# Optimization experiments

Hardware: AMD Instinct MI355X
Metric: run time of the kernel (lower is better)

## Reference

```python
import jax, jax.numpy as jnp
import numpy as np

N = 50000      # nodes
E = 800000     # edges (avg degree 16)
S = 2          # sample_size
D_IN = 128     # input_dim
D_NOISE = 64   # noise_dim
D0 = 256       # output_dims[0]
D1 = 256       # output_dims[1]


def setup_inputs() -> dict:
    key = jax.random.key(0)
    ks = jax.random.split(key, 8)
    X = jax.random.normal(ks[0], (1, N, D_IN), dtype=jnp.float32)
    edge_src = jax.random.randint(ks[1], (E,), 0, N)
    edge_dst = jax.random.randint(ks[2], (E,), 0, N)
    # Bernoulli(0.5) noise, as in torch.distributions.Bernoulli
    epsilon = (jax.random.uniform(ks[3], (S, N, D_NOISE)) < 0.5).astype(jnp.float32)
    W0 = jax.random.normal(ks[4], (D_IN + D_NOISE, D0), dtype=jnp.float32) * 0.05
    b0 = jnp.zeros((D0,), jnp.float32)
    W1 = jax.random.normal(ks[5], (D0, D1), dtype=jnp.float32) * 0.05
    b1 = jnp.zeros((D1,), jnp.float32)
    eps0 = jnp.zeros((), jnp.float32)  # GINConv learnable eps, init 0
    eps1 = jnp.zeros((), jnp.float32)
    return dict(X=X, epsilon=epsilon, edge_src=edge_src, edge_dst=edge_dst,
                W0=W0, b0=b0, W1=W1, b1=b1, eps0=eps0, eps1=eps1)


def reference(X, epsilon, edge_src, edge_dst, W0, b0, W1, b1, eps0, eps1):
    # Expand features over sample dim and concat noise: [S, N, D_IN + D_NOISE]
    feat = jnp.broadcast_to(X, (epsilon.shape[0], X.shape[1], X.shape[2]))
    h = jnp.concatenate([feat, epsilon], axis=2)

    def gin_layer(h, eps, W, b):
        # sum aggregation over in-edges: agg[:, d] += h[:, s] for each edge (s, d)
        agg = jnp.zeros_like(h).at[:, edge_dst, :].add(h[:, edge_src, :])
        return jax.nn.relu(((1.0 + eps) * h + agg) @ W + b)

    h = gin_layer(h, eps0, W0, b0)
    h = gin_layer(h, eps1, W1, b1)
    out = jax.nn.relu(h)  # outer activation applied once more in forward()
    return out, epsilon
```

## Files before the change

kernel.cpp:

```cpp
#include <hip/hip_runtime.h>
#include <hip/hip_bf16.h>

#define NN 50000
#define NE 800000
#define NS 2
#define DIN 128
#define DNOISE 64
#define DH0 192
#define DOUT 256

typedef __bf16 bf16x8 __attribute__((ext_vector_type(8)));
typedef float floatx4 __attribute__((ext_vector_type(4)));


__global__ void count_kernel(const int* __restrict__ dst, int* __restrict__ cnt) {
    int i = blockIdx.x * blockDim.x + threadIdx.x;
    if (i < NE) atomicAdd(&cnt[dst[i]], 1);
}

__global__ __launch_bounds__(1024) void scan_kernel(int* __restrict__ cnt ,
                                                    int* __restrict__ row_ptr) {
    __shared__ int buf[1024];
    __shared__ int carry_s;
    int tid = threadIdx.x;
    if (tid == 0) { carry_s = 0; row_ptr[0] = 0; }
    __syncthreads();
    for (int base = 0; base < NN; base += 1024) {
        int i = base + tid;
        int v = (i < NN) ? cnt[i] : 0;
        buf[tid] = v;
        __syncthreads();
        for (int off = 1; off < 1024; off <<= 1) {
            int t = (tid >= off) ? buf[tid - off] : 0;
            __syncthreads();
            buf[tid] += t;
            __syncthreads();
        }
        int inc = buf[tid] + carry_s;
        if (i < NN) { row_ptr[i + 1] = inc; cnt[i] = inc - v; }
        __syncthreads();
        if (tid == 1023) carry_s = inc;
        __syncthreads();
    }
}

__global__ void fill_kernel(const int* __restrict__ src, const int* __restrict__ dst,
                            int* __restrict__ cursor, int* __restrict__ col_idx) {
    int i = blockIdx.x * blockDim.x + threadIdx.x;
    if (i < NE) {
        int p = atomicAdd(&cursor[dst[i]], 1);
        col_idx[p] = src[i];
    }
}


__global__ void transpose_w(const float* __restrict__ W, __hip_bfloat16* __restrict__ Wt, int K) {
    int n = blockIdx.x;
    for (int k = threadIdx.x; k < K; k += blockDim.x)
        Wt[(size_t)n * K + k] = __float2bfloat16(W[(size_t)k * DOUT + n]);
}


__device__ inline float bflo(unsigned int u) { return __uint_as_float(u << 16); }
__device__ inline float bfhi(unsigned int u) { return __uint_as_float(u & 0xffff0000u); }
__device__ inline unsigned short f2bf_bits(float x) {
    __hip_bfloat16 b = __float2bfloat16(x);
    return *reinterpret_cast<unsigned short*>(&b);
}


__global__ __launch_bounds__(256) void agg0_kernel(
    const float* __restrict__ X, const float* __restrict__ noise,
    const int* __restrict__ row_ptr, const int* __restrict__ col_idx,
    const float* __restrict__ eps0p, __hip_bfloat16* __restrict__ z0) {
    int d = blockIdx.x, tid = threadIdx.x;
    int beg = row_ptr[d], end = row_ptr[d + 1];
    float c = 1.f + eps0p[0];
    if (tid < DIN) {
        const float* src = X + tid;
        float acc = c * src[(size_t)d * DIN];
        int e = beg;
        for (; e + 3 < end; e += 4) {
            int i0 = col_idx[e], i1 = col_idx[e + 1], i2 = col_idx[e + 2], i3 = col_idx[e + 3];
            float v0 = src[(size_t)i0 * DIN], v1 = src[(size_t)i1 * DIN];
            float v2 = src[(size_t)i2 * DIN], v3 = src[(size_t)i3 * DIN];
            acc += (v0 + v1) + (v2 + v3);
        }
        for (; e < end; ++e) acc += src[(size_t)col_idx[e] * DIN];
        __hip_bfloat16 r = __float2bfloat16(acc);
        z0[(size_t)d * DH0 + tid] = r;
        z0[(size_t)(NN + d) * DH0 + tid] = r;
    } else {
        int j = tid - DIN;
        int s = j >> 6, dim = j & 63;
        const float* src = noise + (size_t)s * NN * DNOISE + dim;
        float acc = c * src[(size_t)d * DNOISE];
        int e = beg;
        for (; e + 3 < end; e += 4) {
            int i0 = col_idx[e], i1 = col_idx[e + 1], i2 = col_idx[e + 2], i3 = col_idx[e + 3];
            float v0 = src[(size_t)i0 * DNOISE], v1 = src[(size_t)i1 * DNOISE];
            float v2 = src[(size_t)i2 * DNOISE], v3 = src[(size_t)i3 * DNOISE];
            acc += (v0 + v1) + (v2 + v3);
        }
        for (; e < end; ++e) acc += src[(size_t)col_idx[e] * DNOISE];
        z0[(size_t)(s * NN + d) * DH0 + DIN + dim] = __float2bfloat16(acc);
    }
}


__global__ __launch_bounds__(256) void agg1_kernel(
    const unsigned int* __restrict__ h, const int* __restrict__ row_ptr,
    const int* __restrict__ col_idx, const float* __restrict__ eps1p,
    unsigned int* __restrict__ z1) {
    const int RW = DOUT / 2;
    int d = blockIdx.x, tid = threadIdx.x;
    int s = tid >> 7, cidx = tid & 127;
    int beg = row_ptr[d], end = row_ptr[d + 1];
    float c = 1.f + eps1p[0];
    const unsigned int* src = h + (size_t)s * NN * RW + cidx;
    unsigned int u = src[(size_t)d * RW];
    float aL = c * bflo(u), aH = c * bfhi(u);
    int e = beg;
    for (; e + 3 < end; e += 4) {
        int i0 = col_idx[e], i1 = col_idx[e + 1], i2 = col_idx[e + 2], i3 = col_idx[e + 3];
        unsigned int u0 = src[(size_t)i0 * RW], u1 = src[(size_t)i1 * RW];
        unsigned int u2 = src[(size_t)i2 * RW], u3 = src[(size_t)i3 * RW];
        aL += (bflo(u0) + bflo(u1)) + (bflo(u2) + bflo(u3));
        aH += (bfhi(u0) + bfhi(u1)) + (bfhi(u2) + bfhi(u3));
    }
    for (; e < end; ++e) {
        unsigned int ue = src[(size_t)col_idx[e] * RW];
        aL += bflo(ue); aH += bfhi(ue);
    }
    z1[(size_t)(s * NN + d) * RW + cidx] =
        (unsigned int)f2bf_bits(aL) | ((unsigned int)f2bf_bits(aH) << 16);
}


__device__ inline void store_out(float* C, size_t idx, float v) { C[idx] = v; }
__device__ inline void store_out(__hip_bfloat16* C, size_t idx, float v) { C[idx] = __float2bfloat16(v); }

template <typename OUT_T>
__global__ __launch_bounds__(256) void gemm_bias_relu(
    const __hip_bfloat16* __restrict__ A, const __hip_bfloat16* __restrict__ Wt,
    const float* __restrict__ bias, OUT_T* __restrict__ C,
    int M, int K) {
    const int lane = threadIdx.x & 63;
    const int wave = threadIdx.x >> 6;
    const int rowBase = blockIdx.x * 128 + wave * 32;
    if (rowBase >= M) return;
    const int lo = lane & 15;
    const int quad = lane >> 4;

    floatx4 acc0[16], acc1[16];
#pragma unroll
    for (int t = 0; t < 16; ++t) {
        acc0[t] = (floatx4){0.f, 0.f, 0.f, 0.f};
        acc1[t] = (floatx4){0.f, 0.f, 0.f, 0.f};
    }

    const __hip_bfloat16* arow0 = A + (size_t)(rowBase + lo) * K + quad * 8;
    const __hip_bfloat16* arow1 = arow0 + (size_t)16 * K;
    for (int k0 = 0; k0 < K; k0 += 32) {
        bf16x8 a0 = *reinterpret_cast<const bf16x8*>(arow0 + k0);
        bf16x8 a1 = *reinterpret_cast<const bf16x8*>(arow1 + k0);
#pragma unroll
        for (int t = 0; t < 16; ++t) {
            bf16x8 b = *reinterpret_cast<const bf16x8*>(Wt + (size_t)(t * 16 + lo) * K + k0 + quad * 8);
            acc0[t] = __builtin_amdgcn_mfma_f32_16x16x32_bf16(a0, b, acc0[t], 0, 0, 0);
            acc1[t] = __builtin_amdgcn_mfma_f32_16x16x32_bf16(a1, b, acc1[t], 0, 0, 0);
        }
    }

#pragma unroll
    for (int t = 0; t < 16; ++t) {
        int col = t * 16 + lo;
        float bv = bias[col];
#pragma unroll
        for (int r = 0; r < 4; ++r) {
            int row0 = rowBase + quad * 4 + r;
            float v0 = acc0[t][r] + bv;
            store_out(C, (size_t)row0 * DOUT + col, v0 > 0.f ? v0 : 0.f);
            float v1 = acc1[t][r] + bv;
            store_out(C, (size_t)(row0 + 16) * DOUT + col, v1 > 0.f ? v1 : 0.f);
        }
    }
}


__global__ void copy_eps(const uint4* __restrict__ src, uint4* __restrict__ dst) {
    int i = blockIdx.x * blockDim.x + threadIdx.x;
    const int n16 = (NS * NN * DNOISE * 4) / 16;
    if (i < n16) dst[i] = src[i];
}

extern "C" void kernel_launch(void* const* d_in, const int* in_sizes, int n_in,
                              void* d_out, int out_size, void* d_ws, size_t ws_size,
                              hipStream_t stream) {
    const float* X = (const float*)d_in[0];
    const float* noise = (const float*)d_in[1];
    const int* esrc = (const int*)d_in[2];
    const int* edst = (const int*)d_in[3];
    const float* W0 = (const float*)d_in[4];
    const float* b0 = (const float*)d_in[5];
    const float* W1 = (const float*)d_in[6];
    const float* b1 = (const float*)d_in[7];
    const float* eps0 = (const float*)d_in[8];
    const float* eps1 = (const float*)d_in[9];
    float* out = (float*)d_out;

    char* w = (char*)d_ws;
    auto carve = [&](size_t bytes) { char* p = w; w += (bytes + 511) & ~(size_t)511; return p; };
    int* cursor = (int*)carve((size_t)NN * 4);
    int* row_ptr = (int*)carve((size_t)(NN + 1) * 4);
    int* col_idx = (int*)carve((size_t)NE * 4);
    __hip_bfloat16* Wt0 = (__hip_bfloat16*)carve((size_t)DH0 * DOUT * 2);
    __hip_bfloat16* Wt1 = (__hip_bfloat16*)carve((size_t)DOUT * DOUT * 2);
    __hip_bfloat16* z = (__hip_bfloat16*)carve((size_t)NS * NN * DOUT * 2);
    __hip_bfloat16* h1 = (__hip_bfloat16*)d_out;

    const int M = NS * NN;

    hipMemsetAsync(cursor, 0, (size_t)NN * 4, stream);
    count_kernel<<<(NE + 255) / 256, 256, 0, stream>>>(edst, cursor);
    scan_kernel<<<1, 1024, 0, stream>>>(cursor, row_ptr);
    fill_kernel<<<(NE + 255) / 256, 256, 0, stream>>>(esrc, edst, cursor, col_idx);
    transpose_w<<<DOUT, 256, 0, stream>>>(W0, Wt0, DH0);
    transpose_w<<<DOUT, 256, 0, stream>>>(W1, Wt1, DOUT);

    agg0_kernel<<<NN, 256, 0, stream>>>(X, noise, row_ptr, col_idx, eps0, z);
    gemm_bias_relu<__hip_bfloat16><<<(M + 127) / 128, 256, 0, stream>>>(z, Wt0, b0, h1, M, DH0);
    agg1_kernel<<<NN, 256, 0, stream>>>((const unsigned int*)h1, row_ptr, col_idx, eps1,
                                        (unsigned int*)z);
    gemm_bias_relu<float><<<(M + 127) / 128, 256, 0, stream>>>(z, Wt1, b1, out, M, DOUT);

    copy_eps<<<((NS * NN * DNOISE * 4 / 16) + 255) / 256, 256, 0, stream>>>(
        (const uint4*)noise, (uint4*)(out + (size_t)M * DOUT));
}
```

Baseline: 708.0 us.

## Fuse neighbor aggregation with MFMA GEMM per 32-node tile and gather bf16 inputs

Each GIN layer's aggregation and GEMM are merged into one kernel. A block of 32 nodes gathers neighbor sums for both samples into shared memory, then runs bf16 MFMA with bias and ReLU, so the aggregated intermediate is never written to or read back from global memory. X and the noise are first converted to bf16, using the epsilon output area as scratch, to halve the bytes each gather moves, and the scan now processes four counts per thread. The trade-offs are a serial per-node loop inside each block, which means less parallelism for gathers, and rounding the inputs to bf16 before aggregation.

```diff
diff --git a/kernel.cpp b/kernel.cpp
--- a/kernel.cpp
+++ b/kernel.cpp
@@ -13,6 +13,17 @@
 typedef float floatx4 __attribute__((ext_vector_type(4)));
 
 
+__device__ inline float bflo(unsigned int u) { return __uint_as_float(u << 16); }
+__device__ inline float bfhi(unsigned int u) { return __uint_as_float(u & 0xffff0000u); }
+__device__ inline unsigned short f2bf_bits(float x) {
+    __hip_bfloat16 b = __float2bfloat16(x);
+    return *reinterpret_cast<unsigned short*>(&b);
+}
+__device__ inline unsigned int pack2(float lo, float hi) {
+    return (unsigned int)f2bf_bits(lo) | ((unsigned int)f2bf_bits(hi) << 16);
+}
+
+
 __global__ void count_kernel(const int* __restrict__ dst, int* __restrict__ cnt) {
     int i = blockIdx.x * blockDim.x + threadIdx.x;
     if (i < NE) atomicAdd(&cnt[dst[i]], 1);
@@ -25,10 +36,20 @@
     int tid = threadIdx.x;
     if (tid == 0) { carry_s = 0; row_ptr[0] = 0; }
     __syncthreads();
-    for (int base = 0; base < NN; base += 1024) {
-        int i = base + tid;
-        int v = (i < NN) ? cnt[i] : 0;
-        buf[tid] = v;
+    for (int base = 0; base < NN; base += 4096) {
+        int i = base + tid * 4;
+        int v0 = 0, v1 = 0, v2 = 0, v3 = 0;
+        if (i + 3 < NN) {
+            int4 q = *reinterpret_cast<const int4*>(cnt + i);
+            v0 = q.x; v1 = q.y; v2 = q.z; v3 = q.w;
+        } else {
+            if (i < NN) v0 = cnt[i];
+            if (i + 1 < NN) v1 = cnt[i + 1];
+            if (i + 2 < NN) v2 = cnt[i + 2];
+            if (i + 3 < NN) v3 = cnt[i + 3];
+        }
+        int s = v0 + v1 + v2 + v3;
+        buf[tid] = s;
         __syncthreads();
         for (int off = 1; off < 1024; off <<= 1) {
             int t = (tid >= off) ? buf[tid - off] : 0;
@@ -36,10 +57,14 @@
             buf[tid] += t;
             __syncthreads();
         }
-        int inc = buf[tid] + carry_s;
-        if (i < NN) { row_ptr[i + 1] = inc; cnt[i] = inc - v; }
+        int excl = buf[tid] - s + carry_s;
+        int p1 = excl + v0, p2 = p1 + v1, p3 = p2 + v2, p4 = p3 + v3;
+        if (i < NN)     { cnt[i] = excl;     row_ptr[i + 1] = p1; }
+        if (i + 1 < NN) { cnt[i + 1] = p1;   row_ptr[i + 2] = p2; }
+        if (i + 2 < NN) { cnt[i + 2] = p2;   row_ptr[i + 3] = p3; }
+        if (i + 3 < NN) { cnt[i + 3] = p3;   row_ptr[i + 4] = p4; }
         __syncthreads();
-        if (tid == 1023) carry_s = inc;
+        if (tid == 1023) carry_s = excl + s;
         __syncthreads();
     }
 }
@@ -54,6 +79,17 @@
 }
 
 
+__global__ void tobf16_kernel(const float* __restrict__ src, unsigned short* __restrict__ dst, int n4) {
+    int i = blockIdx.x * blockDim.x + threadIdx.x;
+    if (i < n4) {
+        float4 v = reinterpret_cast<const float4*>(src)[i];
+        ushort4 o;
+        o.x = f2bf_bits(v.x); o.y = f2bf_bits(v.y); o.z = f2bf_bits(v.z); o.w = f2bf_bits(v.w);
+        reinterpret_cast<ushort4*>(dst)[i] = o;
+    }
+}
+
+
 __global__ void transpose_w(const float* __restrict__ W, __hip_bfloat16* __restrict__ Wt, int K) {
     int n = blockIdx.x;
     for (int k = threadIdx.x; k < K; k += blockDim.x)
@@ -61,128 +97,170 @@
 }
 
 
-__device__ inline float bflo(unsigned int u) { return __uint_as_float(u << 16); }
-__device__ inline float bfhi(unsigned int u) { return __uint_as_float(u & 0xffff0000u); }
-__device__ inline unsigned short f2bf_bits(float x) {
-    __hip_bfloat16 b = __float2bfloat16(x);
-    return *reinterpret_cast<unsigned short*>(&b);
-}
-
-
-__global__ __launch_bounds__(256) void agg0_kernel(
-    const float* __restrict__ X, const float* __restrict__ noise,
+__global__ __launch_bounds__(256) void fused0_kernel(
+    const unsigned int* __restrict__ Xb,
+    const unsigned int* __restrict__ Nb,
     const int* __restrict__ row_ptr, const int* __restrict__ col_idx,
-    const float* __restrict__ eps0p, __hip_bfloat16* __restrict__ z0) {
-    int d = blockIdx.x, tid = threadIdx.x;
-    int beg = row_ptr[d], end = row_ptr[d + 1];
-    float c = 1.f + eps0p[0];
-    if (tid < DIN) {
-        const float* src = X + tid;
-        float acc = c * src[(size_t)d * DIN];
+    const float* __restrict__ eps0p,
+    const __hip_bfloat16* __restrict__ Wt0,
+    const float* __restrict__ b0,
+    __hip_bfloat16* __restrict__ h1) {
+    __shared__ unsigned int tile[64][100];
+    const int d0 = blockIdx.x * 32;
+    const int nodes = min(32, NN - d0);
+    const int tid = threadIdx.x;
+    const float c = 1.f + eps0p[0];
+
+    if (nodes < 32 && tid < 100) {
+        for (int r = nodes; r < 32; ++r) { tile[r][tid] = 0; tile[32 + r][tid] = 0; }
+    }
+
+    const int j = tid >> 7;
+    const int cc = tid & 127;
+    for (int it = 0; it < 16; ++it) {
+        int i = it * 2 + j;
+        if (i < nodes) {
+            int d = d0 + i;
+            int beg = row_ptr[d], end = row_ptr[d + 1];
+            if (cc < 64) {
+                const unsigned int* src = Xb + cc;
+                unsigned int u = src[(size_t)d * 64];
+                float aL = c * bflo(u), aH = c * bfhi(u);
+                int e = beg;
+                for (; e + 3 < end; e += 4) {
+                    int i0 = col_idx[e], i1 = col_idx[e + 1], i2 = col_idx[e + 2], i3 = col_idx[e + 3];
+                    unsigned int u0 = src[(size_t)i0 * 64], u1 = src[(size_t)i1 * 64];
+                    unsigned int u2 = src[(size_t)i2 * 64], u3 = src[(size_t)i3 * 64];
+                    aL += (bflo(u0) + bflo(u1)) + (bflo(u2) + bflo(u3));
+                    aH += (bfhi(u0) + bfhi(u1)) + (bfhi(u2) + bfhi(u3));
+                }
+                for (; e < end; ++e) {
+                    unsigned int ue = src[(size_t)col_idx[e] * 64];
+                    aL += bflo(ue); aH += bfhi(ue);
+                }
+                unsigned int r = pack2(aL, aH);
+                tile[i][cc] = r;
+                tile[32 + i][cc] = r;
+            } else {
+                int s = (cc - 64) >> 5, col = (cc - 64) & 31;
+                const unsigned int* src = Nb + (size_t)s * NN * 32 + col;
+                unsigned int u = src[(size_t)d * 32];
+                float aL = c * bflo(u), aH = c * bfhi(u);
+                int e = beg;
+                for (; e + 3 < end; e += 4) {
+                    int i0 = col_idx[e], i1 = col_idx[e + 1], i2 = col_idx[e + 2], i3 = col_idx[e + 3];
+                    unsigned int u0 = src[(size_t)i0 * 32], u1 = src[(size_t)i1 * 32];
+                    unsigned int u2 = src[(size_t)i2 * 32], u3 = src[(size_t)i3 * 32];
+                    aL += (bflo(u0) + bflo(u1)) + (bflo(u2) + bflo(u3));
+                    aH += (bfhi(u0) + bfhi(u1)) + (bfhi(u2) + bfhi(u3));
+                }
+                for (; e < end; ++e) {
+                    unsigned int ue = src[(size_t)col_idx[e] * 32];
+                    aL += bflo(ue); aH += bfhi(ue);
+                }
+                tile[s * 32 + i][64 + col] = pack2(aL, aH);
+            }
+        }
+    }
+    __syncthreads();
+
+    const int lane = tid & 63, w = tid >> 6;
+    const int lo = lane & 15, quad = lane >> 4;
+    floatx4 acc[16];
+#pragma unroll
+    for (int t = 0; t < 16; ++t) acc[t] = (floatx4){0.f, 0.f, 0.f, 0.f};
+    const unsigned int* arow = &tile[w * 16 + lo][0];
+    for (int k0 = 0; k0 < DH0; k0 += 32) {
+        bf16x8 a = *reinterpret_cast<const bf16x8*>(arow + k0 / 2 + quad * 4);
+#pragma unroll
+        for (int t = 0; t < 16; ++t) {
+            bf16x8 b = *reinterpret_cast<const bf16x8*>(Wt0 + (size_t)(t * 16 + lo) * DH0 + k0 + quad * 8);
+            acc[t] = __builtin_amdgcn_mfma_f32_16x16x32_bf16(a, b, acc[t], 0, 0, 0);
+        }
+    }
+#pragma unroll
+    for (int t = 0; t < 16; ++t) {
+        int col = t * 16 + lo;
+        float bv = b0[col];
+#pragma unroll
+        for (int r = 0; r < 4; ++r) {
+            int lr = w * 16 + quad * 4 + r;
+            int i = lr & 31, s = lr >> 5;
+            if (i < nodes) {
+                float v = acc[t][r] + bv;
+                h1[(size_t)(s * NN + d0 + i) * DOUT + col] = __float2bfloat16(v > 0.f ? v : 0.f);
+            }
+        }
+    }
+}
+
+
+__global__ __launch_bounds__(256) void fused1_kernel(
+    const unsigned int* __restrict__ h,
+    const int* __restrict__ row_ptr, const int* __restrict__ col_idx,
+    const float* __restrict__ eps1p,
+    const __hip_bfloat16* __restrict__ Wt1,
+    const float* __restrict__ b1,
+    float* __restrict__ out) {
+    __shared__ unsigned int tile[64][132];
+    const int d0 = blockIdx.x * 32;
+    const int nodes = min(32, NN - d0);
+    const int tid = threadIdx.x;
+    const float c = 1.f + eps1p[0];
+
+    if (nodes < 32 && tid < 132) {
+        for (int r = nodes; r < 32; ++r) { tile[r][tid] = 0; tile[32 + r][tid] = 0; }
+    }
+
+    const int s = tid >> 7, cc = tid & 127;
+    const unsigned int* src = h + (size_t)s * NN * 128 + cc;
+    for (int i = 0; i < nodes; ++i) {
+        int d = d0 + i;
+        int beg = row_ptr[d], end = row_ptr[d + 1];
+        unsigned int u = src[(size_t)d * 128];
+        float aL = c * bflo(u), aH = c * bfhi(u);
         int e = beg;
         for (; e + 3 < end; e += 4) {
             int i0 = col_idx[e], i1 = col_idx[e + 1], i2 = col_idx[e + 2], i3 = col_idx[e + 3];
-            float v0 = src[(size_t)i0 * DIN], v1 = src[(size_t)i1 * DIN];
-            float v2 = src[(size_t)i2 * DIN], v3 = src[(size_t)i3 * DIN];
-            acc += (v0 + v1) + (v2 + v3);
-        }
-        for (; e < end; ++e) acc += src[(size_t)col_idx[e] * DIN];
-        __hip_bfloat16 r = __float2bfloat16(acc);
-        z0[(size_t)d * DH0 + tid] = r;
-        z0[(size_t)(NN + d) * DH0 + tid] = r;
-    } else {
-        int j = tid - DIN;
-        int s = j >> 6, dim = j & 63;
-        const float* src = noise + (size_t)s * NN * DNOISE + dim;
-        float acc = c * src[(size_t)d * DNOISE];
-        int e = beg;
-        for (; e + 3 < end; e += 4) {
-            int i0 = col_idx[e], i1 = col_idx[e + 1], i2 = col_idx[e + 2], i3 = col_idx[e + 3];
-            float v0 = src[(size_t)i0 * DNOISE], v1 = src[(size_t)i1 * DNOISE];
-            float v2 = src[(size_t)i2 * DNOISE], v3 = src[(size_t)i3 * DNOISE];
-            acc += (v0 + v1) + (v2 + v3);
-        }
-        for (; e < end; ++e) acc += src[(size_t)col_idx[e] * DNOISE];
-        z0[(size_t)(s * NN + d) * DH0 + DIN + dim] = __float2bfloat16(acc);
-    }
-}
-
-
-__global__ __launch_bounds__(256) void agg1_kernel(
-    const unsigned int* __restrict__ h, const int* __restrict__ row_ptr,
-    const int* __restrict__ col_idx, const float* __restrict__ eps1p,
-    unsigned int* __restrict__ z1) {
-    const int RW = DOUT / 2;
-    int d = blockIdx.x, tid = threadIdx.x;
-    int s = tid >> 7, cidx = tid & 127;
-    int beg = row_ptr[d], end = row_ptr[d + 1];
-    float c = 1.f + eps1p[0];
-    const unsigned int* src = h + (size_t)s * NN * RW + cidx;
-    unsigned int u = src[(size_t)d * RW];
-    float aL = c * bflo(u), aH = c * bfhi(u);
-    int e = beg;
-    for (; e + 3 < end; e += 4) {
-        int i0 = col_idx[e], i1 = col_idx[e + 1], i2 = col_idx[e + 2], i3 = col_idx[e + 3];
-        unsigned int u0 = src[(size_t)i0 * RW], u1 = src[(size_t)i1 * RW];
-        unsigned int u2 = src[(size_t)i2 * RW], u3 = src[(size_t)i3 * RW];
-        aL += (bflo(u0) + bflo(u1)) + (bflo(u2) + bflo(u3));
-        aH += (bfhi(u0) + bfhi(u1)) + (bfhi(u2) + bfhi(u3));
-    }
-    for (; e < end; ++e) {
-        unsigned int ue = src[(size_t)col_idx[e] * RW];
-        aL += bflo(ue); aH += bfhi(ue);
-    }
-    z1[(size_t)(s * NN + d) * RW + cidx] =
-        (unsigned int)f2bf_bits(aL) | ((unsigned int)f2bf_bits(aH) << 16);
-}
-
-
-__device__ inline void store_out(float* C, size_t idx, float v) { C[idx] = v; }
-__device__ inline void store_out(__hip_bfloat16* C, size_t idx, float v) { C[idx] = __float2bfloat16(v); }
-
-template <typename OUT_T>
-__global__ __launch_bounds__(256) void gemm_bias_relu(
-    const __hip_bfloat16* __restrict__ A, const __hip_bfloat16* __restrict__ Wt,
-    const float* __restrict__ bias, OUT_T* __restrict__ C,
-    int M, int K) {
-    const int lane = threadIdx.x & 63;
-    const int wave = threadIdx.x >> 6;
-    const int rowBase = blockIdx.x * 128 + wave * 32;
-    if (rowBase >= M) return;
-    const int lo = lane & 15;
-    const int quad = lane >> 4;
-
-    floatx4 acc0[16], acc1[16];
-#pragma unroll
-    for (int t = 0; t < 16; ++t) {
-        acc0[t] = (floatx4){0.f, 0.f, 0.f, 0.f};
-        acc1[t] = (floatx4){0.f, 0.f, 0.f, 0.f};
-    }
-
-    const __hip_bfloat16* arow0 = A + (size_t)(rowBase + lo) * K + quad * 8;
-    const __hip_bfloat16* arow1 = arow0 + (size_t)16 * K;
-    for (int k0 = 0; k0 < K; k0 += 32) {
-        bf16x8 a0 = *reinterpret_cast<const bf16x8*>(arow0 + k0);
-        bf16x8 a1 = *reinterpret_cast<const bf16x8*>(arow1 + k0);
+            unsigned int u0 = src[(size_t)i0 * 128], u1 = src[(size_t)i1 * 128];
+            unsigned int u2 = src[(size_t)i2 * 128], u3 = src[(size_t)i3 * 128];
+            aL += (bflo(u0) + bflo(u1)) + (bflo(u2) + bflo(u3));
+            aH += (bfhi(u0) + bfhi(u1)) + (bfhi(u2) + bfhi(u3));
+        }
+        for (; e < end; ++e) {
+            unsigned int ue = src[(size_t)col_idx[e] * 128];
+            aL += bflo(ue); aH += bfhi(ue);
+        }
+        tile[s * 32 + i][cc] = pack2(aL, aH);
+    }
+    __syncthreads();
+
+    const int lane = tid & 63, w = tid >> 6;
+    const int lo = lane & 15, quad = lane >> 4;
+    floatx4 acc[16];
+#pragma unroll
+    for (int t = 0; t < 16; ++t) acc[t] = (floatx4){0.f, 0.f, 0.f, 0.f};
+    const unsigned int* arow = &tile[w * 16 + lo][0];
+    for (int k0 = 0; k0 < DOUT; k0 += 32) {
+        bf16x8 a = *reinterpret_cast<const bf16x8*>(arow + k0 / 2 + quad * 4);
 #pragma unroll
         for (int t = 0; t < 16; ++t) {
-            bf16x8 b = *reinterpret_cast<const bf16x8*>(Wt + (size_t)(t * 16 + lo) * K + k0 + quad * 8);
-            acc0[t] = __builtin_amdgcn_mfma_f32_16x16x32_bf16(a0, b, acc0[t], 0, 0, 0);
-            acc1[t] = __builtin_amdgcn_mfma_f32_16x16x32_bf16(a1, b, acc1[t], 0, 0, 0);
-        }
-    }
-
+            bf16x8 b = *reinterpret_cast<const bf16x8*>(Wt1 + (size_t)(t * 16 + lo) * DOUT + k0 + quad * 8);
+            acc[t] = __builtin_amdgcn_mfma_f32_16x16x32_bf16(a, b, acc[t], 0, 0, 0);
+        }
+    }
 #pragma unroll
     for (int t = 0; t < 16; ++t) {
         int col = t * 16 + lo;
-        float bv = bias[col];
+        float bv = b1[col];
 #pragma unroll
         for (int r = 0; r < 4; ++r) {
-            int row0 = rowBase + quad * 4 + r;
-            float v0 = acc0[t][r] + bv;
-            store_out(C, (size_t)row0 * DOUT + col, v0 > 0.f ? v0 : 0.f);
-            float v1 = acc1[t][r] + bv;
-            store_out(C, (size_t)(row0 + 16) * DOUT + col, v1 > 0.f ? v1 : 0.f);
+            int lr = w * 16 + quad * 4 + r;
+            int i = lr & 31, sp = lr >> 5;
+            if (i < nodes) {
+                float v = acc[t][r] + bv;
+                out[(size_t)(sp * NN + d0 + i) * DOUT + col] = v > 0.f ? v : 0.f;
+            }
         }
     }
 }
@@ -209,6 +287,8 @@
     const float* eps1 = (const float*)d_in[9];
     float* out = (float*)d_out;
 
+    const int M = NS * NN;
+
     char* w = (char*)d_ws;
     auto carve = [&](size_t bytes) { char* p = w; w += (bytes + 511) & ~(size_t)511; return p; };
     int* cursor = (int*)carve((size_t)NN * 4);
@@ -216,23 +296,25 @@
     int* col_idx = (int*)carve((size_t)NE * 4);
     __hip_bfloat16* Wt0 = (__hip_bfloat16*)carve((size_t)DH0 * DOUT * 2);
     __hip_bfloat16* Wt1 = (__hip_bfloat16*)carve((size_t)DOUT * DOUT * 2);
-    __hip_bfloat16* z = (__hip_bfloat16*)carve((size_t)NS * NN * DOUT * 2);
-    __hip_bfloat16* h1 = (__hip_bfloat16*)d_out;
-
-    const int M = NS * NN;
+    __hip_bfloat16* h1 = (__hip_bfloat16*)carve((size_t)M * DOUT * 2);
+
+    unsigned short* Xb = (unsigned short*)(out + (size_t)M * DOUT);
+    unsigned short* Nb = Xb + (size_t)NN * DIN;
 
     hipMemsetAsync(cursor, 0, (size_t)NN * 4, stream);
     count_kernel<<<(NE + 255) / 256, 256, 0, stream>>>(edst, cursor);
     scan_kernel<<<1, 1024, 0, stream>>>(cursor, row_ptr);
     fill_kernel<<<(NE + 255) / 256, 256, 0, stream>>>(esrc, edst, cursor, col_idx);
+    tobf16_kernel<<<(NN * DIN / 4 + 255) / 256, 256, 0, stream>>>(X, Xb, NN * DIN / 4);
+    tobf16_kernel<<<(NS * NN * DNOISE / 4 + 255) / 256, 256, 0, stream>>>(noise, Nb, NS * NN * DNOISE / 4);
     transpose_w<<<DOUT, 256, 0, stream>>>(W0, Wt0, DH0);
     transpose_w<<<DOUT, 256, 0, stream>>>(W1, Wt1, DOUT);
 
-    agg0_kernel<<<NN, 256, 0, stream>>>(X, noise, row_ptr, col_idx, eps0, z);
-    gemm_bias_relu<__hip_bfloat16><<<(M + 127) / 128, 256, 0, stream>>>(z, Wt0, b0, h1, M, DH0);
-    agg1_kernel<<<NN, 256, 0, stream>>>((const unsigned int*)h1, row_ptr, col_idx, eps1,
-                                        (unsigned int*)z);
-    gemm_bias_relu<float><<<(M + 127) / 128, 256, 0, stream>>>(z, Wt1, b1, out, M, DOUT);
+    const int nblocks = (NN + 31) / 32;
+    fused0_kernel<<<nblocks, 256, 0, stream>>>(
+        (const unsigned int*)Xb, (const unsigned int*)Nb, row_ptr, col_idx, eps0, Wt0, b0, h1);
+    fused1_kernel<<<nblocks, 256, 0, stream>>>(
+        (const unsigned int*)h1, row_ptr, col_idx, eps1, Wt1, b1, out);
 
     copy_eps<<<((NS * NN * DNOISE * 4 / 16) + 255) / 256, 256, 0, stream>>>(
         (const uint4*)noise, (uint4*)(out + (size_t)M * DOUT));
```

New measurement: 932.7 us. +31.7%, slower.

## Pre-convert inputs to bf16 and widen per-thread gathers in aggregation kernels

Applied to the files above, without the earlier changes.

Adds kernels that convert X and the noise to bf16 up front, staged in the unused tail of the output buffer, so the layer-0 neighbor gather reads half the bytes per edge and each thread handles two packed columns. The layer-1 gather now loads uint2 (four bf16 values) per thread, and both aggregation kernels process two nodes per block. The scan kernel is also vectorized to four elements per thread so it needs fewer serial iterations. The cost is an extra conversion pass and earlier bf16 rounding of the inputs before summation, which changes numerics slightly.

```diff
diff --git a/kernel.cpp b/kernel.cpp
--- a/kernel.cpp
+++ b/kernel.cpp
@@ -13,6 +13,17 @@
 typedef float floatx4 __attribute__((ext_vector_type(4)));
 
 
+__device__ inline float bflo(unsigned int u) { return __uint_as_float(u << 16); }
+__device__ inline float bfhi(unsigned int u) { return __uint_as_float(u & 0xffff0000u); }
+__device__ inline unsigned short f2bf_bits(float x) {
+    __hip_bfloat16 b = __float2bfloat16(x);
+    return *reinterpret_cast<unsigned short*>(&b);
+}
+__device__ inline unsigned int pack2(float lo, float hi) {
+    return (unsigned int)f2bf_bits(lo) | ((unsigned int)f2bf_bits(hi) << 16);
+}
+
+
 __global__ void count_kernel(const int* __restrict__ dst, int* __restrict__ cnt) {
     int i = blockIdx.x * blockDim.x + threadIdx.x;
     if (i < NE) atomicAdd(&cnt[dst[i]], 1);
@@ -25,10 +36,20 @@
     int tid = threadIdx.x;
     if (tid == 0) { carry_s = 0; row_ptr[0] = 0; }
     __syncthreads();
-    for (int base = 0; base < NN; base += 1024) {
-        int i = base + tid;
-        int v = (i < NN) ? cnt[i] : 0;
-        buf[tid] = v;
+    for (int base = 0; base < NN; base += 4096) {
+        int i = base + tid * 4;
+        int v0 = 0, v1 = 0, v2 = 0, v3 = 0;
+        if (i + 3 < NN) {
+            int4 q = *reinterpret_cast<const int4*>(cnt + i);
+            v0 = q.x; v1 = q.y; v2 = q.z; v3 = q.w;
+        } else {
+            if (i < NN) v0 = cnt[i];
+            if (i + 1 < NN) v1 = cnt[i + 1];
+            if (i + 2 < NN) v2 = cnt[i + 2];
+            if (i + 3 < NN) v3 = cnt[i + 3];
+        }
+        int s = v0 + v1 + v2 + v3;
+        buf[tid] = s;
         __syncthreads();
         for (int off = 1; off < 1024; off <<= 1) {
             int t = (tid >= off) ? buf[tid - off] : 0;
@@ -36,10 +57,14 @@
             buf[tid] += t;
             __syncthreads();
         }
-        int inc = buf[tid] + carry_s;
-        if (i < NN) { row_ptr[i + 1] = inc; cnt[i] = inc - v; }
+        int excl = buf[tid] - s + carry_s;
+        int p1 = excl + v0, p2 = p1 + v1, p3 = p2 + v2, p4 = p3 + v3;
+        if (i < NN)     { cnt[i] = excl;     row_ptr[i + 1] = p1; }
+        if (i + 1 < NN) { cnt[i + 1] = p1;   row_ptr[i + 2] = p2; }
+        if (i + 2 < NN) { cnt[i + 2] = p2;   row_ptr[i + 3] = p3; }
+        if (i + 3 < NN) { cnt[i + 3] = p3;   row_ptr[i + 4] = p4; }
         __syncthreads();
-        if (tid == 1023) carry_s = inc;
+        if (tid == 1023) carry_s = excl + s;
         __syncthreads();
     }
 }
@@ -50,6 +75,17 @@
     if (i < NE) {
         int p = atomicAdd(&cursor[dst[i]], 1);
         col_idx[p] = src[i];
+    }
+}
+
+
+__global__ void tobf16_kernel(const float* __restrict__ src, unsigned short* __restrict__ dst, int n4) {
+    int i = blockIdx.x * blockDim.x + threadIdx.x;
+    if (i < n4) {
+        float4 v = reinterpret_cast<const float4*>(src)[i];
+        ushort4 o;
+        o.x = f2bf_bits(v.x); o.y = f2bf_bits(v.y); o.z = f2bf_bits(v.z); o.w = f2bf_bits(v.w);
+        reinterpret_cast<ushort4*>(dst)[i] = o;
     }
 }
 
@@ -61,79 +97,88 @@
 }
 
 
-__device__ inline float bflo(unsigned int u) { return __uint_as_float(u << 16); }
-__device__ inline float bfhi(unsigned int u) { return __uint_as_float(u & 0xffff0000u); }
-__device__ inline unsigned short f2bf_bits(float x) {
-    __hip_bfloat16 b = __float2bfloat16(x);
-    return *reinterpret_cast<unsigned short*>(&b);
-}
-
-
 __global__ __launch_bounds__(256) void agg0_kernel(
-    const float* __restrict__ X, const float* __restrict__ noise,
+    const unsigned int* __restrict__ Xb,
+    const unsigned int* __restrict__ Nb,
     const int* __restrict__ row_ptr, const int* __restrict__ col_idx,
-    const float* __restrict__ eps0p, __hip_bfloat16* __restrict__ z0) {
-    int d = blockIdx.x, tid = threadIdx.x;
-    int beg = row_ptr[d], end = row_ptr[d + 1];
-    float c = 1.f + eps0p[0];
-    if (tid < DIN) {
-        const float* src = X + tid;
-        float acc = c * src[(size_t)d * DIN];
+    const float* __restrict__ eps0p,
+    unsigned int* __restrict__ z0) {
+    const int d = blockIdx.x * 2 + (threadIdx.x >> 7);
+    const int cc = threadIdx.x & 127;
+    const float c = 1.f + eps0p[0];
+    const int beg = row_ptr[d], end = row_ptr[d + 1];
+    if (cc < 64) {
+        const unsigned int* src = Xb + cc;
+        unsigned int u = src[(size_t)d * 64];
+        float aL = c * bflo(u), aH = c * bfhi(u);
         int e = beg;
         for (; e + 3 < end; e += 4) {
             int i0 = col_idx[e], i1 = col_idx[e + 1], i2 = col_idx[e + 2], i3 = col_idx[e + 3];
-            float v0 = src[(size_t)i0 * DIN], v1 = src[(size_t)i1 * DIN];
-            float v2 = src[(size_t)i2 * DIN], v3 = src[(size_t)i3 * DIN];
-            acc += (v0 + v1) + (v2 + v3);
-        }
-        for (; e < end; ++e) acc += src[(size_t)col_idx[e] * DIN];
-        __hip_bfloat16 r = __float2bfloat16(acc);
-        z0[(size_t)d * DH0 + tid] = r;
-        z0[(size_t)(NN + d) * DH0 + tid] = r;
+            unsigned int u0 = src[(size_t)i0 * 64], u1 = src[(size_t)i1 * 64];
+            unsigned int u2 = src[(size_t)i2 * 64], u3 = src[(size_t)i3 * 64];
+            aL += (bflo(u0) + bflo(u1)) + (bflo(u2) + bflo(u3));
+            aH += (bfhi(u0) + bfhi(u1)) + (bfhi(u2) + bfhi(u3));
+        }
+        for (; e < end; ++e) {
+            unsigned int ue = src[(size_t)col_idx[e] * 64];
+            aL += bflo(ue); aH += bfhi(ue);
+        }
+        unsigned int r = pack2(aL, aH);
+        z0[(size_t)d * 96 + cc] = r;
+        z0[(size_t)(NN + d) * 96 + cc] = r;
     } else {
-        int j = tid - DIN;
-        int s = j >> 6, dim = j & 63;
-        const float* src = noise + (size_t)s * NN * DNOISE + dim;
-        float acc = c * src[(size_t)d * DNOISE];
+        int s = (cc - 64) >> 5, col = (cc - 64) & 31;
+        const unsigned int* src = Nb + (size_t)s * NN * 32 + col;
+        unsigned int u = src[(size_t)d * 32];
+        float aL = c * bflo(u), aH = c * bfhi(u);
         int e = beg;
         for (; e + 3 < end; e += 4) {
             int i0 = col_idx[e], i1 = col_idx[e + 1], i2 = col_idx[e + 2], i3 = col_idx[e + 3];
-            float v0 = src[(size_t)i0 * DNOISE], v1 = src[(size_t)i1 * DNOISE];
-            float v2 = src[(size_t)i2 * DNOISE], v3 = src[(size_t)i3 * DNOISE];
-            acc += (v0 + v1) + (v2 + v3);
-        }
-        for (; e < end; ++e) acc += src[(size_t)col_idx[e] * DNOISE];
-        z0[(size_t)(s * NN + d) * DH0 + DIN + dim] = __float2bfloat16(acc);
+            unsigned int u0 = src[(size_t)i0 * 32], u1 = src[(size_t)i1 * 32];
+            unsigned int u2 = src[(size_t)i2 * 32], u3 = src[(size_t)i3 * 32];
+            aL += (bflo(u0) + bflo(u1)) + (bflo(u2) + bflo(u3));
+            aH += (bfhi(u0) + bfhi(u1)) + (bfhi(u2) + bfhi(u3));
+        }
+        for (; e < end; ++e) {
+            unsigned int ue = src[(size_t)col_idx[e] * 32];
+            aL += bflo(ue); aH += bfhi(ue);
+        }
+        z0[(size_t)(s * NN + d) * 96 + 64 + col] = pack2(aL, aH);
     }
 }
 
 
 __global__ __launch_bounds__(256) void agg1_kernel(
-    const unsigned int* __restrict__ h, const int* __restrict__ row_ptr,
-    const int* __restrict__ col_idx, const float* __restrict__ eps1p,
-    unsigned int* __restrict__ z1) {
-    const int RW = DOUT / 2;
-    int d = blockIdx.x, tid = threadIdx.x;
-    int s = tid >> 7, cidx = tid & 127;
-    int beg = row_ptr[d], end = row_ptr[d + 1];
-    float c = 1.f + eps1p[0];
-    const unsigned int* src = h + (size_t)s * NN * RW + cidx;
-    unsigned int u = src[(size_t)d * RW];
-    float aL = c * bflo(u), aH = c * bfhi(u);
+    const uint2* __restrict__ h,
+    const int* __restrict__ row_ptr, const int* __restrict__ col_idx,
+    const float* __restrict__ eps1p,
+    uint2* __restrict__ z1) {
+    const int d = blockIdx.x * 2 + (threadIdx.x >> 7);
+    const int s = (threadIdx.x >> 6) & 1;
+    const int cc = threadIdx.x & 63;
+    const float c = 1.f + eps1p[0];
+    const int beg = row_ptr[d], end = row_ptr[d + 1];
+    const uint2* src = h + (size_t)s * NN * 64 + cc;
+    uint2 u = src[(size_t)d * 64];
+    float aL0 = c * bflo(u.x), aH0 = c * bfhi(u.x);
+    float aL1 = c * bflo(u.y), aH1 = c * bfhi(u.y);
     int e = beg;
     for (; e + 3 < end; e += 4) {
         int i0 = col_idx[e], i1 = col_idx[e + 1], i2 = col_idx[e + 2], i3 = col_idx[e + 3];
-        unsigned int u0 = src[(size_t)i0 * RW], u1 = src[(size_t)i1 * RW];
-        unsigned int u2 = src[(size_t)i2 * RW], u3 = src[(size_t)i3 * RW];
-        aL += (bflo(u0) + bflo(u1)) + (bflo(u2) + bflo(u3));
-        aH += (bfhi(u0) + bfhi(u1)) + (bfhi(u2) + bfhi(u3));
+        uint2 u0 = src[(size_t)i0 * 64], u1 = src[(size_t)i1 * 64];
+        uint2 u2 = src[(size_t)i2 * 64], u3 = src[(size_t)i3 * 64];
+        aL0 += (bflo(u0.x) + bflo(u1.x)) + (bflo(u2.x) + bflo(u3.x));
+        aH0 += (bfhi(u0.x) + bfhi(u1.x)) + (bfhi(u2.x) + bfhi(u3.x));
+        aL1 += (bflo(u0.y) + bflo(u1.y)) + (bflo(u2.y) + bflo(u3.y));
+        aH1 += (bfhi(u0.y) + bfhi(u1.y)) + (bfhi(u2.y) + bfhi(u3.y));
     }
     for (; e < end; ++e) {
-        unsigned int ue = src[(size_t)col_idx[e] * RW];
-        aL += bflo(ue); aH += bfhi(ue);
-    }
-    z1[(size_t)(s * NN + d) * RW + cidx] =
-        (unsigned int)f2bf_bits(aL) | ((unsigned int)f2bf_bits(aH) << 16);
+        uint2 ue = src[(size_t)col_idx[e] * 64];
+        aL0 += bflo(ue.x); aH0 += bfhi(ue.x);
+        aL1 += bflo(ue.y); aH1 += bfhi(ue.y);
+    }
+    uint2 r; r.x = pack2(aL0, aH0); r.y = pack2(aL1, aH1);
+    z1[(size_t)(s * NN + d) * 64 + cc] = r;
 }
 
 
@@ -209,6 +254,8 @@
     const float* eps1 = (const float*)d_in[9];
     float* out = (float*)d_out;
 
+    const int M = NS * NN;
+
     char* w = (char*)d_ws;
     auto carve = [&](size_t bytes) { char* p = w; w += (bytes + 511) & ~(size_t)511; return p; };
     int* cursor = (int*)carve((size_t)NN * 4);
@@ -216,23 +263,29 @@
     int* col_idx = (int*)carve((size_t)NE * 4);
     __hip_bfloat16* Wt0 = (__hip_bfloat16*)carve((size_t)DH0 * DOUT * 2);
     __hip_bfloat16* Wt1 = (__hip_bfloat16*)carve((size_t)DOUT * DOUT * 2);
-    __hip_bfloat16* z = (__hip_bfloat16*)carve((size_t)NS * NN * DOUT * 2);
+    unsigned int* z = (unsigned int*)carve((size_t)M * DOUT * 2);
+
     __hip_bfloat16* h1 = (__hip_bfloat16*)d_out;
-
-    const int M = NS * NN;
+    unsigned short* Xb = (unsigned short*)(out + (size_t)M * DOUT);
+    unsigned short* Nb = Xb + (size_t)NN * DIN;
 
     hipMemsetAsync(cursor, 0, (size_t)NN * 4, stream);
     count_kernel<<<(NE + 255) / 256, 256, 0, stream>>>(edst, cursor);
     scan_kernel<<<1, 1024, 0, stream>>>(cursor, row_ptr);
     fill_kernel<<<(NE + 255) / 256, 256, 0, stream>>>(esrc, edst, cursor, col_idx);
+    tobf16_kernel<<<(NN * DIN / 4 + 255) / 256, 256, 0, stream>>>(X, Xb, NN * DIN / 4);
+    tobf16_kernel<<<(NS * NN * DNOISE / 4 + 255) / 256, 256, 0, stream>>>(noise, Nb, NS * NN * DNOISE / 4);
     transpose_w<<<DOUT, 256, 0, stream>>>(W0, Wt0, DH0);
     transpose_w<<<DOUT, 256, 0, stream>>>(W1, Wt1, DOUT);
 
-    agg0_kernel<<<NN, 256, 0, stream>>>(X, noise, row_ptr, col_idx, eps0, z);
-    gemm_bias_relu<__hip_bfloat16><<<(M + 127) / 128, 256, 0, stream>>>(z, Wt0, b0, h1, M, DH0);
-    agg1_kernel<<<NN, 256, 0, stream>>>((const unsigned int*)h1, row_ptr, col_idx, eps1,
-                                        (unsigned int*)z);
-    gemm_bias_relu<float><<<(M + 127) / 128, 256, 0, stream>>>(z, Wt1, b1, out, M, DOUT);
+    agg0_kernel<<<NN / 2, 256, 0, stream>>>(
+        (const unsigned int*)Xb, (const unsigned int*)Nb, row_ptr, col_idx, eps0, z);
+    gemm_bias_relu<__hip_bfloat16><<<(M + 127) / 128, 256, 0, stream>>>(
+        (const __hip_bfloat16*)z, Wt0, b0, h1, M, DH0);
+    agg1_kernel<<<NN / 2, 256, 0, stream>>>(
+        (const uint2*)h1, row_ptr, col_idx, eps1, (uint2*)z);
+    gemm_bias_relu<float><<<(M + 127) / 128, 256, 0, stream>>>(
+        (const __hip_bfloat16*)z, Wt1, b1, out, M, DOUT);
 
     copy_eps<<<((NS * NN * DNOISE * 4 / 16) + 255) / 256, 256, 0, stream>>>(
         (const uint4*)noise, (uint4*)(out + (size_t)M * DOUT));
```

New measurement: 620.8 us. 12.3% less time.
